# Kernel optimization log

Measured on AMD Instinct MI355X. Metric: run time of the kernel, lower is better.

The kernel has to match this reference:

```python
import jax, jax.numpy as jnp
import numpy as np

NL, D, DI, N, R, K = 32, 256, 512, 16, 16, 4   # layers, d_model, d_inner, d_state, dt_rank, d_conv
V, FF, BATCH, L = 4096, 1024, 32, 256


def _mamba_layer(x, p):
    # x: (B, L, D). One pre-norm Mamba block with residual: x + mamba(LN(x)).
    ln_w, ln_b, in_w, cw, cb, xp_w, dtw, dtb, A_log, Dskip, out_w = p
    mu = x.mean(-1, keepdims=True)
    var = ((x - mu) ** 2).mean(-1, keepdims=True)
    h = (x - mu) / jnp.sqrt(var + 1e-5) * ln_w + ln_b
    xz = jnp.einsum('bld,ed->ble', h, in_w)            # (B, L, 2*DI)
    xm, z = jnp.split(xz, 2, axis=-1)
    seq = xm.shape[1]
    # causal depthwise conv1d, kernel K, then SiLU
    xpad = jnp.pad(xm, ((0, 0), (K - 1, 0), (0, 0)))
    xc = sum(xpad[:, k:k + seq] * cw[:, k] for k in range(K)) + cb
    xc = jax.nn.silu(xc)
    dbc = jnp.einsum('ble,fe->blf', xc, xp_w)          # (B, L, R+2N)
    dt, Bm, Cm = jnp.split(dbc, [R, R + N], axis=-1)
    dt = jax.nn.softplus(jnp.einsum('blr,er->ble', dt, dtw) + dtb)  # (B, L, DI)
    A = -jnp.exp(A_log)                                # (DI, N)

    def step(hs, inp):
        dt_t, B_t, C_t, x_t = inp                      # (B,DI),(B,N),(B,N),(B,DI)
        dA = jnp.exp(dt_t[..., None] * A)              # (B, DI, N)
        hs = hs * dA + (dt_t * x_t)[..., None] * B_t[:, None, :]
        return hs, jnp.einsum('ben,bn->be', hs, C_t)

    h0 = jnp.zeros((xc.shape[0], DI, N), xc.dtype)
    _, ys = jax.lax.scan(step, h0, (dt.swapaxes(0, 1), Bm.swapaxes(0, 1), Cm.swapaxes(0, 1), xc.swapaxes(0, 1)))
    y = ys.swapaxes(0, 1) + xc * Dskip
    y = y * jax.nn.silu(z)
    return x + jnp.einsum('ble,de->bld', y, out_w)


def _stack_forward(x, params):
    return jax.lax.scan(lambda c, p: (jax.checkpoint(_mamba_layer)(c, p), None), x, params)[0]


def setup_inputs() -> dict:
    key = jax.random.key(0)
    ks = jax.random.split(key, 12)
    rn = lambda k, shape, s=0.02: jax.random.normal(k, shape, jnp.float32) * s
    return {
        'token_ids': jax.random.randint(ks[0], (BATCH, L), 0, V),
        'emb': rn(ks[1], (V, D)),
        'ln_w': jnp.ones((NL, D)), 'ln_b': jnp.zeros((NL, D)),
        'in_proj_w': rn(ks[2], (NL, 2 * DI, D)),
        'conv_w': rn(ks[3], (NL, DI, K), 0.1), 'conv_b': jnp.zeros((NL, DI)),
        'x_proj_w': rn(ks[4], (NL, R + 2 * N, DI)),
        'dt_w': rn(ks[5], (NL, DI, R), 0.1),
        'dt_b': jnp.full((NL, DI), float(np.log(np.expm1(0.01))), jnp.float32),
        'A_log': jnp.broadcast_to(jnp.log(jnp.arange(1, N + 1, dtype=jnp.float32)), (NL, DI, N)) + 0.0,
        'Dskip': jnp.ones((NL, DI)),
        'out_proj_w': rn(ks[6], (NL, D, DI)),
        'W1': rn(ks[7], (FF, D)), 'b1': jnp.zeros((FF,)),
        'W2': rn(ks[8], (V, FF)), 'b2': jnp.zeros((V,)),
    }


def reference(token_ids, emb, ln_w, ln_b, in_proj_w, conv_w, conv_b, x_proj_w, dt_w, dt_b, A_log, Dskip, out_proj_w, W1, b1, W2, b2):
    x = emb[token_ids]                                  # (B, L, D)
    params = (ln_w, ln_b, in_proj_w, conv_w, conv_b, x_proj_w, dt_w, dt_b, A_log, Dskip, out_proj_w)
    x = _stack_forward(x, params)                       # 32 stacked Mamba blocks
    h = jax.nn.relu(x @ W1.T + b1)
    return h @ W2.T + b2                                # (B, L, V) logits
```

## Files before the change

kernel.cpp:

```cpp
#include <hip/hip_runtime.h>
#include <hip/hip_bf16.h>
#include <cstdint>
#include <cstddef>


typedef __bf16 v8bf __attribute__((ext_vector_type(8)));
typedef float  v4f  __attribute__((ext_vector_type(4)));

__device__ __forceinline__ void async_copy16(const void* g, void* l) {
  __builtin_amdgcn_global_load_lds((const __attribute__((address_space(1))) void*)g,
                                   (__attribute__((address_space(3))) void*)l, 16, 0, 0);
}

__device__ __forceinline__ float bf(__bf16 v) { return (float)v; }

constexpr size_t OFF_WIN  = 0;
constexpr size_t OFF_WXP  = 16777216;
constexpr size_t OFF_WOUT = 18350080;
constexpr size_t OFF_WW1  = 26738688;
constexpr size_t OFF_WW2  = 27262976;
constexpr size_t OFF_X    = 35651584;
constexpr size_t OFF_H    = 44040192;
constexpr size_t OFF_XZ   = 48234496;
constexpr size_t OFF_XC   = 65011712;
constexpr size_t OFF_DBC  = 73400320;
constexpr size_t OFF_Y    = 74973184;
constexpr size_t OFF_PART = 83361792;
constexpr size_t OFF_PROD = 91750400;

__global__ __launch_bounds__(256)
void f2b_multi(const float* __restrict__ s0, const float* __restrict__ s1,
               const float* __restrict__ s2, const float* __restrict__ s3,
               const float* __restrict__ s4, char* __restrict__ ws) {
  size_t i = (size_t)blockIdx.x * 256 + threadIdx.x;
  if (i < 8388608) { ((__bf16*)(ws + OFF_WIN))[i] = (__bf16)s0[i]; return; }
  i -= 8388608;
  if (i < 786432)  { ((__bf16*)(ws + OFF_WXP))[i] = (__bf16)s1[i]; return; }
  i -= 786432;
  if (i < 4194304) { ((__bf16*)(ws + OFF_WOUT))[i] = (__bf16)s2[i]; return; }
  i -= 4194304;
  if (i < 262144)  { ((__bf16*)(ws + OFF_WW1))[i] = (__bf16)s3[i]; return; }
  i -= 262144;
  ((__bf16*)(ws + OFF_WW2))[i] = (__bf16)s4[i];
}

__global__ __launch_bounds__(256) void f2b_k(const float* __restrict__ X,
                                             __bf16* __restrict__ O) {
  size_t i = (size_t)blockIdx.x * 256 + threadIdx.x;
  O[i] = (__bf16)X[i];
}

__global__ __launch_bounds__(256)
void embed_ln_k(const int* __restrict__ tok, const float* __restrict__ emb,
                const float* __restrict__ w, const float* __restrict__ b,
                float* __restrict__ X, __bf16* __restrict__ H) {
  int row = blockIdx.x;
  int t   = threadIdx.x;
  float v = emb[(size_t)tok[row] * 256 + t];
  X[(size_t)row * 256 + t] = v;
  float s = v, q = v * v;
  #pragma unroll
  for (int o = 32; o > 0; o >>= 1) { s += __shfl_xor(s, o); q += __shfl_xor(q, o); }
  __shared__ float ss[4], qq[4];
  int wv = t >> 6;
  if ((t & 63) == 0) { ss[wv] = s; qq[wv] = q; }
  __syncthreads();
  s = ss[0] + ss[1] + ss[2] + ss[3];
  q = qq[0] + qq[1] + qq[2] + qq[3];
  float mu  = s * (1.f / 256.f);
  float var = q * (1.f / 256.f) - mu * mu;
  float r   = rsqrtf(var + 1e-5f);
  H[(size_t)row * 256 + t] = (__bf16)((v - mu) * r * w[t] + b[t]);
}

template <int EPI>
__global__ __launch_bounds__(256, 2)
void gemm_bt(const __bf16* __restrict__ A, const __bf16* __restrict__ W,
             void* outp, const float* __restrict__ bias, int M, int N, int K) {
  __shared__ __align__(16) __bf16 sA[128 * 32];
  __shared__ __align__(16) __bf16 sB[128 * 32];
  const int tid  = threadIdx.x;
  const int bm0  = blockIdx.y << 7;
  const int bn0  = blockIdx.x << 7;
  const int lane = tid & 63;
  const int wv   = tid >> 6;
  const int wm   = (wv >> 1) << 6;
  const int wn   = (wv & 1) << 6;
  const int lr   = lane & 15;
  const int lk   = lane >> 4;

  v4f acc[4][4] = {};

  const int r0 = tid >> 2;
  const int c0 = (tid & 3) << 3;
  const int wbase = (tid & ~63) << 3;

  const __bf16* gA0 = A + (size_t)(bm0 + r0) * K + c0;
  const __bf16* gA1 = A + (size_t)(bm0 + 64 + r0) * K + c0;
  const __bf16* gB0 = W + (size_t)(bn0 + r0) * K + c0;
  const __bf16* gB1 = W + (size_t)(bn0 + 64 + r0) * K + c0;

  for (int kk = 0; kk < K; kk += 32) {
    async_copy16(gA0 + kk, sA + wbase);
    async_copy16(gA1 + kk, sA + 2048 + wbase);
    async_copy16(gB0 + kk, sB + wbase);
    async_copy16(gB1 + kk, sB + 2048 + wbase);
    __syncthreads();
    v8bf af[4], bfr[4];
    #pragma unroll
    for (int i = 0; i < 4; ++i)
      af[i] = *(const v8bf*)(sA + ((wm + i * 16 + lr) << 5) + (lk << 3));
    #pragma unroll
    for (int j = 0; j < 4; ++j)
      bfr[j] = *(const v8bf*)(sB + ((wn + j * 16 + lr) << 5) + (lk << 3));
    #pragma unroll
    for (int i = 0; i < 4; ++i)
      #pragma unroll
      for (int j = 0; j < 4; ++j)
        acc[i][j] = __builtin_amdgcn_mfma_f32_16x16x32_bf16(af[i], bfr[j], acc[i][j], 0, 0, 0);
    __syncthreads();
  }

  #pragma unroll
  for (int i = 0; i < 4; ++i) {
    #pragma unroll
    for (int j = 0; j < 4; ++j) {
      int gc = bn0 + wn + j * 16 + lr;
      #pragma unroll
      for (int v = 0; v < 4; ++v) {
        int gr = bm0 + wm + i * 16 + (lk << 2) + v;
        float val = acc[i][j][v];
        size_t idx = (size_t)gr * N + gc;
        if (EPI == 0) {
          ((__bf16*)outp)[idx] = (__bf16)val;
        } else if (EPI == 1) {
          val += bias[gc]; val = fmaxf(val, 0.f);
          ((__bf16*)outp)[idx] = (__bf16)val;
        } else {
          ((float*)outp)[idx] = val + bias[gc];
        }
      }
    }
  }
}

__global__ __launch_bounds__(192, 2)
void convxproj_k(const __bf16* __restrict__ XZ, const float* __restrict__ cw,
                 const float* __restrict__ cb, const __bf16* __restrict__ Wxp,
                 __bf16* __restrict__ XC, float* __restrict__ DBC) {
  __shared__ __align__(16) __bf16 sA[32 * 32];
  __shared__ __align__(16) __bf16 sB[48 * 32];
  const int tid  = threadIdx.x;
  const int bl0  = blockIdx.x << 5;
  const int lane = tid & 63, wv = tid >> 6;
  const int lr = lane & 15, lk = lane >> 4;
  v4f acc[2] = {};

  const int ar = tid >> 2;
  const int ac = (tid & 3) << 3;
  const int bl = bl0 + ar;
  const int l  = bl & 255;

  for (int kk = 0; kk < 512; kk += 32) {
    async_copy16(Wxp + (size_t)(tid >> 2) * 512 + ((tid & 3) << 3) + kk,
                 sB + ((tid & ~63) << 3));
    if (tid < 128) {
      const int e = kk + ac;
      float a[8];
      #pragma unroll
      for (int j = 0; j < 8; ++j) a[j] = cb[e + j];
      #pragma unroll
      for (int k = 0; k < 4; ++k) {
        if (l + k >= 3) {
          const v8bf xv = *(const v8bf*)(XZ + (size_t)(bl + k - 3) * 1024 + e);
          #pragma unroll
          for (int j = 0; j < 8; ++j) a[j] += bf(xv[j]) * cw[(e + j) * 4 + k];
        }
      }
      v8bf outv;
      #pragma unroll
      for (int j = 0; j < 8; ++j) {
        float s = a[j] / (1.f + __expf(-a[j]));
        outv[j] = (__bf16)s;
      }
      *(v8bf*)(sA + ar * 32 + ac) = outv;
      *(v8bf*)(XC + (size_t)bl * 512 + e) = outv;
    }
    __syncthreads();
    v8bf af[2], bfr;
    #pragma unroll
    for (int i = 0; i < 2; ++i)
      af[i] = *(const v8bf*)(sA + ((i * 16 + lr) << 5) + (lk << 3));
    bfr = *(const v8bf*)(sB + ((wv * 16 + lr) << 5) + (lk << 3));
    #pragma unroll
    for (int i = 0; i < 2; ++i)
      acc[i] = __builtin_amdgcn_mfma_f32_16x16x32_bf16(af[i], bfr, acc[i], 0, 0, 0);
    __syncthreads();
  }
  const int gc = wv * 16 + lr;
  #pragma unroll
  for (int i = 0; i < 2; ++i)
    #pragma unroll
    for (int v = 0; v < 4; ++v) {
      int gr = bl0 + i * 16 + (lk << 2) + v;
      DBC[(size_t)gr * 48 + gc] = acc[i][v];
    }
}

__global__ __launch_bounds__(256, 2)
void scan_pass1(const float* __restrict__ DBC, const __bf16* __restrict__ XC,
                const float* __restrict__ dtw, const float* __restrict__ dtb,
                const float* __restrict__ Alog,
                float* __restrict__ PART, float* __restrict__ PROD) {
  const int e = blockIdx.x * 256 + threadIdx.x;
  const int b = blockIdx.y;
  const int c = blockIdx.z;
  float Arow[16], Wdt[16];
  #pragma unroll
  for (int n = 0; n < 16; ++n) {
    Arow[n] = -__expf(Alog[e * 16 + n]);
    Wdt[n]  = dtw[e * 16 + n];
  }
  const float bias = dtb[e];
  float part[16], prod[16];
  #pragma unroll
  for (int n = 0; n < 16; ++n) { part[n] = 0.f; prod[n] = 1.f; }
  const int bl0 = b * 256 + c * 32;
  for (int tt = 0; tt < 32; ++tt) {
    const v4f* dp = (const v4f*)(DBC + (size_t)(bl0 + tt) * 48);
    v4f d0 = dp[0], d1 = dp[1], d2 = dp[2], d3 = dp[3];
    v4f bv0 = dp[4], bv1 = dp[5], bv2 = dp[6], bv3 = dp[7];
    float dtv = bias;
    #pragma unroll
    for (int r = 0; r < 4; ++r)
      dtv += d0[r] * Wdt[r] + d1[r] * Wdt[r + 4] + d2[r] * Wdt[r + 8] + d3[r] * Wdt[r + 12];
    dtv = (dtv > 20.f) ? dtv : log1pf(__expf(dtv));
    float x = bf(XC[(size_t)(bl0 + tt) * 512 + e]);
    float dtx = dtv * x;
    float Bv[16];
    #pragma unroll
    for (int r = 0; r < 4; ++r) { Bv[r] = bv0[r]; Bv[r+4] = bv1[r]; Bv[r+8] = bv2[r]; Bv[r+12] = bv3[r]; }
    #pragma unroll
    for (int n = 0; n < 16; ++n) {
      float dA = __expf(dtv * Arow[n]);
      part[n] = part[n] * dA + dtx * Bv[n];
      prod[n] *= dA;
    }
  }
  size_t o = (((size_t)c * 32 + b) * 512 + e) * 16;
  #pragma unroll
  for (int n = 0; n < 16; ++n) { PART[o + n] = part[n]; PROD[o + n] = prod[n]; }
}

__global__ __launch_bounds__(256, 2)
void scan_pass2(const float* __restrict__ DBC, const __bf16* __restrict__ XC,
                const __bf16* __restrict__ XZ,
                const float* __restrict__ dtw, const float* __restrict__ dtb,
                const float* __restrict__ Alog, const float* __restrict__ Dskip,
                const float* __restrict__ PART, const float* __restrict__ PROD,
                __bf16* __restrict__ Y) {
  const int e = blockIdx.x * 256 + threadIdx.x;
  const int b = blockIdx.y;
  const int c = blockIdx.z;
  float Arow[16], Wdt[16];
  #pragma unroll
  for (int n = 0; n < 16; ++n) {
    Arow[n] = -__expf(Alog[e * 16 + n]);
    Wdt[n]  = dtw[e * 16 + n];
  }
  const float bias = dtb[e];
  const float Dsk  = Dskip[e];
  float h[16];
  #pragma unroll
  for (int n = 0; n < 16; ++n) h[n] = 0.f;
  for (int cc = 0; cc < c; ++cc) {
    size_t o = (((size_t)cc * 32 + b) * 512 + e) * 16;
    const v4f* pp = (const v4f*)(PART + o);
    const v4f* qq = (const v4f*)(PROD + o);
    #pragma unroll
    for (int r = 0; r < 4; ++r) {
      v4f p = pp[r], q = qq[r];
      #pragma unroll
      for (int v = 0; v < 4; ++v) h[r * 4 + v] = q[v] * h[r * 4 + v] + p[v];
    }
  }
  const int bl0 = b * 256 + c * 32;
  for (int tt = 0; tt < 32; ++tt) {
    const v4f* dp = (const v4f*)(DBC + (size_t)(bl0 + tt) * 48);
    v4f d0 = dp[0], d1 = dp[1], d2 = dp[2], d3 = dp[3];
    v4f bv0 = dp[4], bv1 = dp[5], bv2 = dp[6], bv3 = dp[7];
    v4f cv0 = dp[8], cv1 = dp[9], cv2 = dp[10], cv3 = dp[11];
    float dtv = bias;
    #pragma unroll
    for (int r = 0; r < 4; ++r)
      dtv += d0[r] * Wdt[r] + d1[r] * Wdt[r + 4] + d2[r] * Wdt[r + 8] + d3[r] * Wdt[r + 12];
    dtv = (dtv > 20.f) ? dtv : log1pf(__expf(dtv));
    float x = bf(XC[(size_t)(bl0 + tt) * 512 + e]);
    float dtx = dtv * x;
    float Bv[16], Cv[16];
    #pragma unroll
    for (int r = 0; r < 4; ++r) {
      Bv[r] = bv0[r]; Bv[r+4] = bv1[r]; Bv[r+8] = bv2[r]; Bv[r+12] = bv3[r];
      Cv[r] = cv0[r]; Cv[r+4] = cv1[r]; Cv[r+8] = cv2[r]; Cv[r+12] = cv3[r];
    }
    float y = 0.f;
    #pragma unroll
    for (int n = 0; n < 16; ++n) {
      float dA = __expf(dtv * Arow[n]);
      h[n] = h[n] * dA + dtx * Bv[n];
      y += h[n] * Cv[n];
    }
    float z  = bf(XZ[(size_t)(bl0 + tt) * 1024 + 512 + e]);
    float sg = z / (1.f + __expf(-z));
    Y[(size_t)(bl0 + tt) * 512 + e] = (__bf16)((y + x * Dsk) * sg);
  }
}

__global__ __launch_bounds__(256, 2)
void gemm_out_ln_k(const __bf16* __restrict__ Yb, const __bf16* __restrict__ Wout,
                   const float* __restrict__ lnw, const float* __restrict__ lnb,
                   float* __restrict__ X, __bf16* __restrict__ H) {
  __shared__ __align__(16) __bf16 sA[32 * 32];
  __shared__ __align__(16) __bf16 sB[256 * 32];
  __shared__ float sSum[4][32], sSq[4][32];
  const int tid  = threadIdx.x;
  const int bm0  = blockIdx.x << 5;
  const int lane = tid & 63, wv = tid >> 6;
  const int lr = lane & 15, lk = lane >> 4;
  v4f acc[2][4] = {};

  const int ar = tid >> 2;
  const int ac = (tid & 3) << 3;

  for (int kk = 0; kk < 512; kk += 32) {
    if (tid < 128)
      async_copy16(Yb + (size_t)(bm0 + ar) * 512 + ac + kk, sA + ((tid & ~63) << 3));
    #pragma unroll
    for (int j = 0; j < 4; ++j) {
      int ch = j * 256 + tid;
      async_copy16(Wout + (size_t)(ch >> 2) * 512 + ((ch & 3) << 3) + kk,
                   sB + ((j * 256 + (tid & ~63)) << 3));
    }
    __syncthreads();
    v8bf af[2], bfr[4];
    #pragma unroll
    for (int i = 0; i < 2; ++i)
      af[i] = *(const v8bf*)(sA + ((i * 16 + lr) << 5) + (lk << 3));
    #pragma unroll
    for (int j = 0; j < 4; ++j)
      bfr[j] = *(const v8bf*)(sB + ((wv * 64 + j * 16 + lr) << 5) + (lk << 3));
    #pragma unroll
    for (int i = 0; i < 2; ++i)
      #pragma unroll
      for (int j = 0; j < 4; ++j)
        acc[i][j] = __builtin_amdgcn_mfma_f32_16x16x32_bf16(af[i], bfr[j], acc[i][j], 0, 0, 0);
    __syncthreads();
  }

  float s2[2][4], q2[2][4];
  #pragma unroll
  for (int i = 0; i < 2; ++i)
    #pragma unroll
    for (int v = 0; v < 4; ++v) {
      int gr = bm0 + i * 16 + (lk << 2) + v;
      float s = 0.f, q = 0.f;
      #pragma unroll
      for (int j = 0; j < 4; ++j) {
        int gc = wv * 64 + j * 16 + lr;
        float val = X[(size_t)gr * 256 + gc] + acc[i][j][v];
        acc[i][j][v] = val;
        s += val; q += val * val;
      }
      #pragma unroll
      for (int o = 8; o > 0; o >>= 1) { s += __shfl_xor(s, o); q += __shfl_xor(q, o); }
      s2[i][v] = s; q2[i][v] = q;
    }
  if (lr == 0) {
    #pragma unroll
    for (int i = 0; i < 2; ++i)
      #pragma unroll
      for (int v = 0; v < 4; ++v) {
        int row = i * 16 + (lk << 2) + v;
        sSum[wv][row] = s2[i][v];
        sSq[wv][row]  = q2[i][v];
      }
  }
  __syncthreads();
  #pragma unroll
  for (int i = 0; i < 2; ++i)
    #pragma unroll
    for (int v = 0; v < 4; ++v) {
      int row = i * 16 + (lk << 2) + v;
      float S = sSum[0][row] + sSum[1][row] + sSum[2][row] + sSum[3][row];
      float Q = sSq[0][row]  + sSq[1][row]  + sSq[2][row]  + sSq[3][row];
      float mu  = S * (1.f / 256.f);
      float var = Q * (1.f / 256.f) - mu * mu;
      float rinv = rsqrtf(var + 1e-5f);
      int gr = bm0 + row;
      #pragma unroll
      for (int j = 0; j < 4; ++j) {
        int gc = wv * 64 + j * 16 + lr;
        float val = acc[i][j][v];
        X[(size_t)gr * 256 + gc] = val;
        H[(size_t)gr * 256 + gc] = (__bf16)((val - mu) * rinv * lnw[gc] + lnb[gc]);
      }
    }
}

extern "C" void kernel_launch(void* const* d_in, const int* in_sizes, int n_in,
                              void* d_out, int out_size, void* d_ws, size_t ws_size,
                              hipStream_t stream) {
  const int*   tok  = (const int*)d_in[0];
  const float* emb  = (const float*)d_in[1];
  const float* lnw  = (const float*)d_in[2];
  const float* lnb  = (const float*)d_in[3];
  const float* inw  = (const float*)d_in[4];
  const float* cw   = (const float*)d_in[5];
  const float* cb   = (const float*)d_in[6];
  const float* xpw  = (const float*)d_in[7];
  const float* dtw  = (const float*)d_in[8];
  const float* dtb  = (const float*)d_in[9];
  const float* alog = (const float*)d_in[10];
  const float* dsk  = (const float*)d_in[11];
  const float* outw = (const float*)d_in[12];
  const float* W1   = (const float*)d_in[13];
  const float* b1   = (const float*)d_in[14];
  const float* W2   = (const float*)d_in[15];
  const float* b2   = (const float*)d_in[16];

  char* ws = (char*)d_ws;
  __bf16* WIN  = (__bf16*)(ws + OFF_WIN);
  __bf16* WXP  = (__bf16*)(ws + OFF_WXP);
  __bf16* WOUT = (__bf16*)(ws + OFF_WOUT);
  __bf16* WW1  = (__bf16*)(ws + OFF_WW1);
  __bf16* WW2  = (__bf16*)(ws + OFF_WW2);
  float*  X    = (float*)(ws + OFF_X);
  __bf16* H    = (__bf16*)(ws + OFF_H);
  __bf16* XZ   = (__bf16*)(ws + OFF_XZ);
  __bf16* XC   = (__bf16*)(ws + OFF_XC);
  float*  DBC  = (float*)(ws + OFF_DBC);
  __bf16* Y    = (__bf16*)(ws + OFF_Y);
  float*  PART = (float*)(ws + OFF_PART);
  float*  PROD = (float*)(ws + OFF_PROD);
  __bf16* XB   = (__bf16*)(ws + OFF_PART);
  __bf16* HH   = (__bf16*)(ws + OFF_PROD);

  f2b_multi<<<69632, 256, 0, stream>>>(inw, xpw, outw, W1, W2, ws);
  embed_ln_k<<<8192, 256, 0, stream>>>(tok, emb, lnw, lnb, X, H);

  for (int l = 0; l < 32; ++l) {
    const __bf16* inw_l  = WIN  + (size_t)l * 1024 * 256;
    const float*  cw_l   = cw   + (size_t)l * 512 * 4;
    const float*  cb_l   = cb   + (size_t)l * 512;
    const __bf16* xpw_l  = WXP  + (size_t)l * 48 * 512;
    const float*  dtw_l  = dtw  + (size_t)l * 512 * 16;
    const float*  dtb_l  = dtb  + (size_t)l * 512;
    const float*  alog_l = alog + (size_t)l * 512 * 16;
    const float*  dsk_l  = dsk  + (size_t)l * 512;
    const __bf16* outw_l = WOUT + (size_t)l * 256 * 512;
    const int lnx = (l + 1 < 32) ? l + 1 : 31;

    gemm_bt<0><<<dim3(8, 64), 256, 0, stream>>>(H, inw_l, XZ, nullptr, 8192, 1024, 256);
    convxproj_k<<<256, 192, 0, stream>>>(XZ, cw_l, cb_l, xpw_l, XC, DBC);
    scan_pass1<<<dim3(2, 32, 7), 256, 0, stream>>>(DBC, XC, dtw_l, dtb_l, alog_l, PART, PROD);
    scan_pass2<<<dim3(2, 32, 8), 256, 0, stream>>>(DBC, XC, XZ, dtw_l, dtb_l, alog_l, dsk_l,
                                                   PART, PROD, Y);
    gemm_out_ln_k<<<256, 256, 0, stream>>>(Y, outw_l, lnw + (size_t)lnx * 256,
                                           lnb + (size_t)lnx * 256, X, H);
  }

  f2b_k<<<8192, 256, 0, stream>>>(X, XB);
  gemm_bt<1><<<dim3(8, 64), 256, 0, stream>>>(XB, WW1, HH, b1, 8192, 1024, 256);
  gemm_bt<2><<<dim3(32, 64), 256, 0, stream>>>(HH, WW2, (float*)d_out, b2, 8192, 4096, 1024);
}
```

Baseline: 4.926 ms.

## Fuse conv+xproj+scan pass1 and scan pass2+out-proj+LN into two kernels

Result: faster. 4.236 ms (-14.0%).

```diff
diff --git a/kernel.cpp b/kernel.cpp
--- a/kernel.cpp
+++ b/kernel.cpp
@@ -22,9 +22,7 @@
 constexpr size_t OFF_X    = 35651584;
 constexpr size_t OFF_H    = 44040192;
 constexpr size_t OFF_XZ   = 48234496;
-constexpr size_t OFF_XC   = 65011712;
 constexpr size_t OFF_DBC  = 73400320;
-constexpr size_t OFF_Y    = 74973184;
 constexpr size_t OFF_PART = 83361792;
 constexpr size_t OFF_PROD = 91750400;
 
@@ -144,149 +142,182 @@
   }
 }
 
-__global__ __launch_bounds__(192, 2)
-void convxproj_k(const __bf16* __restrict__ XZ, const float* __restrict__ cw,
-                 const float* __restrict__ cb, const __bf16* __restrict__ Wxp,
-                 __bf16* __restrict__ XC, float* __restrict__ DBC) {
-  __shared__ __align__(16) __bf16 sA[32 * 32];
-  __shared__ __align__(16) __bf16 sB[48 * 32];
-  const int tid  = threadIdx.x;
-  const int bl0  = blockIdx.x << 5;
-  const int lane = tid & 63, wv = tid >> 6;
-  const int lr = lane & 15, lk = lane >> 4;
-  v4f acc[2] = {};
-
-  const int ar = tid >> 2;
-  const int ac = (tid & 3) << 3;
-  const int bl = bl0 + ar;
-  const int l  = bl & 255;
-
-  for (int kk = 0; kk < 512; kk += 32) {
-    async_copy16(Wxp + (size_t)(tid >> 2) * 512 + ((tid & 3) << 3) + kk,
-                 sB + ((tid & ~63) << 3));
-    if (tid < 128) {
-      const int e = kk + ac;
+__global__ __launch_bounds__(512, 2)
+void convscan1_k(const __bf16* __restrict__ XZ,
+                 const float* __restrict__ cw, const float* __restrict__ cb,
+                 const __bf16* __restrict__ Wxp,
+                 const float* __restrict__ dtw, const float* __restrict__ dtb,
+                 const float* __restrict__ Alog,
+                 float* __restrict__ DBC,
+                 float* __restrict__ PART, float* __restrict__ PROD) {
+  __shared__ __align__(16) __bf16 sXC[32 * 512];
+  __shared__ __align__(16) float  sDBC[32 * 48];
+  const int tid = threadIdx.x;
+  const int c   = blockIdx.x >> 5;
+  const int b   = blockIdx.x & 31;
+  const int bl0 = b * 256 + c * 32;
+
+  {
+    const int r  = tid >> 4;
+    const int ec = tid & 15;
+    #pragma unroll
+    for (int j = 0; j < 4; ++j) {
+      const int e = (ec << 3) + (j << 7);
+      v4f cw4[8];
+      #pragma unroll
+      for (int jj = 0; jj < 8; ++jj) cw4[jj] = *(const v4f*)(cw + (size_t)(e + jj) * 4);
       float a[8];
       #pragma unroll
-      for (int j = 0; j < 8; ++j) a[j] = cb[e + j];
+      for (int jj = 0; jj < 8; ++jj) a[jj] = cb[e + jj];
       #pragma unroll
       for (int k = 0; k < 4; ++k) {
-        if (l + k >= 3) {
-          const v8bf xv = *(const v8bf*)(XZ + (size_t)(bl + k - 3) * 1024 + e);
+        if (c > 0 || r + k >= 3) {
+          const v8bf xv = *(const v8bf*)(XZ + (size_t)(bl0 + r + k - 3) * 1024 + e);
           #pragma unroll
-          for (int j = 0; j < 8; ++j) a[j] += bf(xv[j]) * cw[(e + j) * 4 + k];
+          for (int jj = 0; jj < 8; ++jj) a[jj] += bf(xv[jj]) * cw4[jj][k];
         }
       }
       v8bf outv;
       #pragma unroll
-      for (int j = 0; j < 8; ++j) {
-        float s = a[j] / (1.f + __expf(-a[j]));
-        outv[j] = (__bf16)s;
+      for (int jj = 0; jj < 8; ++jj) {
+        float s = a[jj] / (1.f + __expf(-a[jj]));
+        outv[jj] = (__bf16)s;
       }
-      *(v8bf*)(sA + ar * 32 + ac) = outv;
-      *(v8bf*)(XC + (size_t)bl * 512 + e) = outv;
-    }
-    __syncthreads();
-    v8bf af[2], bfr;
+      const int cbk = (e >> 3) ^ (r & 7);
+      *(v8bf*)(sXC + r * 512 + (cbk << 3)) = outv;
+    }
+  }
+  __syncthreads();
+
+  if (tid < 192) {
+    const int w = tid >> 6, lane = tid & 63, lr = lane & 15, lk = lane >> 4;
+    v4f acc[2] = {};
+    for (int kk = 0; kk < 512; kk += 32) {
+      const v8bf bfr = *(const v8bf*)(Wxp + (size_t)(w * 16 + lr) * 512 + kk + (lk << 3));
+      #pragma unroll
+      for (int i = 0; i < 2; ++i) {
+        const int row = i * 16 + lr;
+        const int cbk = (((kk >> 3) + lk) ^ (row & 7));
+        const v8bf af = *(const v8bf*)(sXC + row * 512 + (cbk << 3));
+        acc[i] = __builtin_amdgcn_mfma_f32_16x16x32_bf16(af, bfr, acc[i], 0, 0, 0);
+      }
+    }
+    const int gc = w * 16 + lr;
     #pragma unroll
     for (int i = 0; i < 2; ++i)
-      af[i] = *(const v8bf*)(sA + ((i * 16 + lr) << 5) + (lk << 3));
-    bfr = *(const v8bf*)(sB + ((wv * 16 + lr) << 5) + (lk << 3));
-    #pragma unroll
-    for (int i = 0; i < 2; ++i)
-      acc[i] = __builtin_amdgcn_mfma_f32_16x16x32_bf16(af[i], bfr, acc[i], 0, 0, 0);
-    __syncthreads();
-  }
-  const int gc = wv * 16 + lr;
-  #pragma unroll
-  for (int i = 0; i < 2; ++i)
-    #pragma unroll
-    for (int v = 0; v < 4; ++v) {
-      int gr = bl0 + i * 16 + (lk << 2) + v;
-      DBC[(size_t)gr * 48 + gc] = acc[i][v];
-    }
-}
-
-__global__ __launch_bounds__(256, 2)
-void scan_pass1(const float* __restrict__ DBC, const __bf16* __restrict__ XC,
-                const float* __restrict__ dtw, const float* __restrict__ dtb,
-                const float* __restrict__ Alog,
-                float* __restrict__ PART, float* __restrict__ PROD) {
-  const int e = blockIdx.x * 256 + threadIdx.x;
-  const int b = blockIdx.y;
-  const int c = blockIdx.z;
-  float Arow[16], Wdt[16];
-  #pragma unroll
-  for (int n = 0; n < 16; ++n) {
-    Arow[n] = -__expf(Alog[e * 16 + n]);
-    Wdt[n]  = dtw[e * 16 + n];
-  }
-  const float bias = dtb[e];
-  float part[16], prod[16];
-  #pragma unroll
-  for (int n = 0; n < 16; ++n) { part[n] = 0.f; prod[n] = 1.f; }
-  const int bl0 = b * 256 + c * 32;
-  for (int tt = 0; tt < 32; ++tt) {
-    const v4f* dp = (const v4f*)(DBC + (size_t)(bl0 + tt) * 48);
-    v4f d0 = dp[0], d1 = dp[1], d2 = dp[2], d3 = dp[3];
-    v4f bv0 = dp[4], bv1 = dp[5], bv2 = dp[6], bv3 = dp[7];
-    float dtv = bias;
-    #pragma unroll
-    for (int r = 0; r < 4; ++r)
-      dtv += d0[r] * Wdt[r] + d1[r] * Wdt[r + 4] + d2[r] * Wdt[r + 8] + d3[r] * Wdt[r + 12];
-    dtv = (dtv > 20.f) ? dtv : log1pf(__expf(dtv));
-    float x = bf(XC[(size_t)(bl0 + tt) * 512 + e]);
-    float dtx = dtv * x;
-    float Bv[16];
-    #pragma unroll
-    for (int r = 0; r < 4; ++r) { Bv[r] = bv0[r]; Bv[r+4] = bv1[r]; Bv[r+8] = bv2[r]; Bv[r+12] = bv3[r]; }
+      #pragma unroll
+      for (int v = 0; v < 4; ++v)
+        sDBC[(i * 16 + (lk << 2) + v) * 48 + gc] = acc[i][v];
+  }
+  __syncthreads();
+
+  if (tid < 384)
+    *(v4f*)(DBC + (size_t)bl0 * 48 + tid * 4) = *(const v4f*)(sDBC + tid * 4);
+
+  if (c < 7) {
+    const int e = tid;
+    float Arow2[16], Wdt[16];
     #pragma unroll
     for (int n = 0; n < 16; ++n) {
-      float dA = __expf(dtv * Arow[n]);
-      part[n] = part[n] * dA + dtx * Bv[n];
-      prod[n] *= dA;
-    }
-  }
-  size_t o = (((size_t)c * 32 + b) * 512 + e) * 16;
-  #pragma unroll
-  for (int n = 0; n < 16; ++n) { PART[o + n] = part[n]; PROD[o + n] = prod[n]; }
-}
-
-__global__ __launch_bounds__(256, 2)
-void scan_pass2(const float* __restrict__ DBC, const __bf16* __restrict__ XC,
-                const __bf16* __restrict__ XZ,
+      Arow2[n] = -1.4426950408889634f * __expf(Alog[(size_t)e * 16 + n]);
+      Wdt[n]   = dtw[(size_t)e * 16 + n];
+    }
+    const float bias = dtb[e];
+    float part[16], prod[16];
+    #pragma unroll
+    for (int n = 0; n < 16; ++n) { part[n] = 0.f; prod[n] = 1.f; }
+    for (int tt = 0; tt < 32; ++tt) {
+      const v4f* dp = (const v4f*)(sDBC + tt * 48);
+      v4f d0 = dp[0], d1 = dp[1], d2 = dp[2], d3 = dp[3];
+      v4f bv0 = dp[4], bv1 = dp[5], bv2 = dp[6], bv3 = dp[7];
+      float dtv = bias;
+      #pragma unroll
+      for (int r = 0; r < 4; ++r)
+        dtv += d0[r] * Wdt[r] + d1[r] * Wdt[r + 4] + d2[r] * Wdt[r + 8] + d3[r] * Wdt[r + 12];
+      dtv = (dtv > 20.f) ? dtv : log1pf(__expf(dtv));
+      const float x = bf(sXC[tt * 512 + (((e >> 3) ^ (tt & 7)) << 3) + (e & 7)]);
+      const float dtx = dtv * x;
+      float Bv[16];
+      #pragma unroll
+      for (int r = 0; r < 4; ++r) { Bv[r] = bv0[r]; Bv[r+4] = bv1[r]; Bv[r+8] = bv2[r]; Bv[r+12] = bv3[r]; }
+      #pragma unroll
+      for (int n = 0; n < 16; ++n) {
+        const float dA = exp2f(dtv * Arow2[n]);
+        part[n] = part[n] * dA + dtx * Bv[n];
+        prod[n] *= dA;
+      }
+    }
+    const size_t o = (((size_t)c * 32 + b) * 512 + e) * 16;
+    #pragma unroll
+    for (int rq = 0; rq < 4; ++rq) {
+      v4f p, q;
+      #pragma unroll
+      for (int v = 0; v < 4; ++v) { p[v] = part[rq * 4 + v]; q[v] = prod[rq * 4 + v]; }
+      *(v4f*)(PART + o + rq * 4) = p;
+      *(v4f*)(PROD + o + rq * 4) = q;
+    }
+  }
+}
+
+__global__ __launch_bounds__(512, 2)
+void scan2out_k(const __bf16* __restrict__ XZ,
+                const float* __restrict__ cw, const float* __restrict__ cb,
+                const float* __restrict__ DBC,
                 const float* __restrict__ dtw, const float* __restrict__ dtb,
                 const float* __restrict__ Alog, const float* __restrict__ Dskip,
                 const float* __restrict__ PART, const float* __restrict__ PROD,
-                __bf16* __restrict__ Y) {
-  const int e = blockIdx.x * 256 + threadIdx.x;
-  const int b = blockIdx.y;
-  const int c = blockIdx.z;
-  float Arow[16], Wdt[16];
+                const __bf16* __restrict__ Wout,
+                const float* __restrict__ lnw, const float* __restrict__ lnb,
+                float* __restrict__ X, __bf16* __restrict__ H) {
+  __shared__ __align__(16) __bf16 sY[32 * 520];
+  __shared__ __align__(16) __bf16 sB[256 * 32];
+  __shared__ float sSum[4][32], sSq[4][32];
+  const int tid = threadIdx.x;
+  const int c   = blockIdx.x >> 5;
+  const int b   = blockIdx.x & 31;
+  const int bl0 = b * 256 + c * 32;
+  const int e   = tid;
+
+  float Arow2[16], Wdt[16];
   #pragma unroll
   for (int n = 0; n < 16; ++n) {
-    Arow[n] = -__expf(Alog[e * 16 + n]);
-    Wdt[n]  = dtw[e * 16 + n];
+    Arow2[n] = -1.4426950408889634f * __expf(Alog[(size_t)e * 16 + n]);
+    Wdt[n]   = dtw[(size_t)e * 16 + n];
   }
   const float bias = dtb[e];
   const float Dsk  = Dskip[e];
+  const v4f   cwv  = *(const v4f*)(cw + (size_t)e * 4);
+  const float cbe  = cb[e];
+
   float h[16];
   #pragma unroll
   for (int n = 0; n < 16; ++n) h[n] = 0.f;
   for (int cc = 0; cc < c; ++cc) {
-    size_t o = (((size_t)cc * 32 + b) * 512 + e) * 16;
-    const v4f* pp = (const v4f*)(PART + o);
-    const v4f* qq = (const v4f*)(PROD + o);
-    #pragma unroll
-    for (int r = 0; r < 4; ++r) {
-      v4f p = pp[r], q = qq[r];
-      #pragma unroll
-      for (int v = 0; v < 4; ++v) h[r * 4 + v] = q[v] * h[r * 4 + v] + p[v];
-    }
-  }
-  const int bl0 = b * 256 + c * 32;
+    const size_t o = (((size_t)cc * 32 + b) * 512 + e) * 16;
+    #pragma unroll
+    for (int rq = 0; rq < 4; ++rq) {
+      const v4f p = *(const v4f*)(PART + o + rq * 4);
+      const v4f q = *(const v4f*)(PROD + o + rq * 4);
+      #pragma unroll
+      for (int v = 0; v < 4; ++v) h[rq * 4 + v] = q[v] * h[rq * 4 + v] + p[v];
+    }
+  }
+
+  float w0 = 0.f, w1 = 0.f, w2 = 0.f;
+  if (c > 0) {
+    w0 = bf(XZ[(size_t)(bl0 - 3) * 1024 + e]);
+    w1 = bf(XZ[(size_t)(bl0 - 2) * 1024 + e]);
+    w2 = bf(XZ[(size_t)(bl0 - 1) * 1024 + e]);
+  }
+
+  #pragma unroll 2
   for (int tt = 0; tt < 32; ++tt) {
-    const v4f* dp = (const v4f*)(DBC + (size_t)(bl0 + tt) * 48);
+    const float xt = bf(XZ[(size_t)(bl0 + tt) * 1024 + e]);
+    float a = cbe + w0 * cwv[0] + w1 * cwv[1] + w2 * cwv[2] + xt * cwv[3];
+    const float x = a / (1.f + __expf(-a));
+    w0 = w1; w1 = w2; w2 = xt;
+    const float* dpf = DBC + (size_t)(bl0 + tt) * 48;
+    const v4f* dp = (const v4f*)dpf;
     v4f d0 = dp[0], d1 = dp[1], d2 = dp[2], d3 = dp[3];
     v4f bv0 = dp[4], bv1 = dp[5], bv2 = dp[6], bv3 = dp[7];
     v4f cv0 = dp[8], cv1 = dp[9], cv2 = dp[10], cv3 = dp[11];
@@ -295,8 +326,7 @@
     for (int r = 0; r < 4; ++r)
       dtv += d0[r] * Wdt[r] + d1[r] * Wdt[r + 4] + d2[r] * Wdt[r + 8] + d3[r] * Wdt[r + 12];
     dtv = (dtv > 20.f) ? dtv : log1pf(__expf(dtv));
-    float x = bf(XC[(size_t)(bl0 + tt) * 512 + e]);
-    float dtx = dtv * x;
+    const float dtx = dtv * x;
     float Bv[16], Cv[16];
     #pragma unroll
     for (int r = 0; r < 4; ++r) {
@@ -306,105 +336,77 @@
     float y = 0.f;
     #pragma unroll
     for (int n = 0; n < 16; ++n) {
-      float dA = __expf(dtv * Arow[n]);
+      const float dA = exp2f(dtv * Arow2[n]);
       h[n] = h[n] * dA + dtx * Bv[n];
       y += h[n] * Cv[n];
     }
-    float z  = bf(XZ[(size_t)(bl0 + tt) * 1024 + 512 + e]);
-    float sg = z / (1.f + __expf(-z));
-    Y[(size_t)(bl0 + tt) * 512 + e] = (__bf16)((y + x * Dsk) * sg);
-  }
-}
-
-__global__ __launch_bounds__(256, 2)
-void gemm_out_ln_k(const __bf16* __restrict__ Yb, const __bf16* __restrict__ Wout,
-                   const float* __restrict__ lnw, const float* __restrict__ lnb,
-                   float* __restrict__ X, __bf16* __restrict__ H) {
-  __shared__ __align__(16) __bf16 sA[32 * 32];
-  __shared__ __align__(16) __bf16 sB[256 * 32];
-  __shared__ float sSum[4][32], sSq[4][32];
-  const int tid  = threadIdx.x;
-  const int bm0  = blockIdx.x << 5;
-  const int lane = tid & 63, wv = tid >> 6;
-  const int lr = lane & 15, lk = lane >> 4;
-  v4f acc[2][4] = {};
-
-  const int ar = tid >> 2;
-  const int ac = (tid & 3) << 3;
-
+    const float z  = bf(XZ[(size_t)(bl0 + tt) * 1024 + 512 + e]);
+    const float sg = z / (1.f + __expf(-z));
+    sY[tt * 520 + e] = (__bf16)((y + x * Dsk) * sg);
+  }
+  __syncthreads();
+
+  const int w = tid >> 6, lane = tid & 63, lr = lane & 15, lk = lane >> 4;
+  const int wm = (w & 1) << 4;
+  const int wn = (w >> 1) << 6;
+  v4f acc[4] = {};
   for (int kk = 0; kk < 512; kk += 32) {
-    if (tid < 128)
-      async_copy16(Yb + (size_t)(bm0 + ar) * 512 + ac + kk, sA + ((tid & ~63) << 3));
+    async_copy16(Wout + (size_t)(tid >> 2) * 512 + ((tid & 3) << 3) + kk,
+                 sB + ((tid & ~63) << 3));
+    async_copy16(Wout + (size_t)(128 + (tid >> 2)) * 512 + ((tid & 3) << 3) + kk,
+                 sB + 4096 + ((tid & ~63) << 3));
+    __syncthreads();
+    const v8bf af = *(const v8bf*)(sY + (wm + lr) * 520 + kk + (lk << 3));
     #pragma unroll
     for (int j = 0; j < 4; ++j) {
-      int ch = j * 256 + tid;
-      async_copy16(Wout + (size_t)(ch >> 2) * 512 + ((ch & 3) << 3) + kk,
-                   sB + ((j * 256 + (tid & ~63)) << 3));
+      const v8bf bfr = *(const v8bf*)(sB + ((wn + j * 16 + lr) << 5) + (lk << 3));
+      acc[j] = __builtin_amdgcn_mfma_f32_16x16x32_bf16(af, bfr, acc[j], 0, 0, 0);
     }
     __syncthreads();
-    v8bf af[2], bfr[4];
-    #pragma unroll
-    for (int i = 0; i < 2; ++i)
-      af[i] = *(const v8bf*)(sA + ((i * 16 + lr) << 5) + (lk << 3));
-    #pragma unroll
-    for (int j = 0; j < 4; ++j)
-      bfr[j] = *(const v8bf*)(sB + ((wv * 64 + j * 16 + lr) << 5) + (lk << 3));
-    #pragma unroll
-    for (int i = 0; i < 2; ++i)
-      #pragma unroll
-      for (int j = 0; j < 4; ++j)
-        acc[i][j] = __builtin_amdgcn_mfma_f32_16x16x32_bf16(af[i], bfr[j], acc[i][j], 0, 0, 0);
-    __syncthreads();
-  }
-
-  float s2[2][4], q2[2][4];
-  #pragma unroll
-  for (int i = 0; i < 2; ++i)
+  }
+
+  float s2[4], q2[4];
+  #pragma unroll
+  for (int v = 0; v < 4; ++v) {
+    const int gr = bl0 + wm + (lk << 2) + v;
+    float s = 0.f, q = 0.f;
+    #pragma unroll
+    for (int j = 0; j < 4; ++j) {
+      const int gc = wn + j * 16 + lr;
+      float val = X[(size_t)gr * 256 + gc] + acc[j][v];
+      acc[j][v] = val;
+      s += val; q += val * val;
+    }
+    #pragma unroll
+    for (int o = 8; o > 0; o >>= 1) { s += __shfl_xor(s, o); q += __shfl_xor(q, o); }
+    s2[v] = s; q2[v] = q;
+  }
+  if (lr == 0) {
     #pragma unroll
     for (int v = 0; v < 4; ++v) {
-      int gr = bm0 + i * 16 + (lk << 2) + v;
-      float s = 0.f, q = 0.f;
-      #pragma unroll
-      for (int j = 0; j < 4; ++j) {
-        int gc = wv * 64 + j * 16 + lr;
-        float val = X[(size_t)gr * 256 + gc] + acc[i][j][v];
-        acc[i][j][v] = val;
-        s += val; q += val * val;
-      }
-      #pragma unroll
-      for (int o = 8; o > 0; o >>= 1) { s += __shfl_xor(s, o); q += __shfl_xor(q, o); }
-      s2[i][v] = s; q2[i][v] = q;
-    }
-  if (lr == 0) {
-    #pragma unroll
-    for (int i = 0; i < 2; ++i)
-      #pragma unroll
-      for (int v = 0; v < 4; ++v) {
-        int row = i * 16 + (lk << 2) + v;
-        sSum[wv][row] = s2[i][v];
-        sSq[wv][row]  = q2[i][v];
-      }
+      const int row = wm + (lk << 2) + v;
+      sSum[w >> 1][row] = s2[v];
+      sSq[w >> 1][row]  = q2[v];
+    }
   }
   __syncthreads();
   #pragma unroll
-  for (int i = 0; i < 2; ++i)
-    #pragma unroll
-    for (int v = 0; v < 4; ++v) {
-      int row = i * 16 + (lk << 2) + v;
-      float S = sSum[0][row] + sSum[1][row] + sSum[2][row] + sSum[3][row];
-      float Q = sSq[0][row]  + sSq[1][row]  + sSq[2][row]  + sSq[3][row];
-      float mu  = S * (1.f / 256.f);
-      float var = Q * (1.f / 256.f) - mu * mu;
-      float rinv = rsqrtf(var + 1e-5f);
-      int gr = bm0 + row;
-      #pragma unroll
-      for (int j = 0; j < 4; ++j) {
-        int gc = wv * 64 + j * 16 + lr;
-        float val = acc[i][j][v];
-        X[(size_t)gr * 256 + gc] = val;
-        H[(size_t)gr * 256 + gc] = (__bf16)((val - mu) * rinv * lnw[gc] + lnb[gc]);
-      }
-    }
+  for (int v = 0; v < 4; ++v) {
+    const int row = wm + (lk << 2) + v;
+    const float S = sSum[0][row] + sSum[1][row] + sSum[2][row] + sSum[3][row];
+    const float Q = sSq[0][row]  + sSq[1][row]  + sSq[2][row]  + sSq[3][row];
+    const float mu  = S * (1.f / 256.f);
+    const float var = Q * (1.f / 256.f) - mu * mu;
+    const float rinv = rsqrtf(var + 1e-5f);
+    const int gr = bl0 + row;
+    #pragma unroll
+    for (int j = 0; j < 4; ++j) {
+      const int gc = wn + j * 16 + lr;
+      const float val = acc[j][v];
+      X[(size_t)gr * 256 + gc] = val;
+      H[(size_t)gr * 256 + gc] = (__bf16)((val - mu) * rinv * lnw[gc] + lnb[gc]);
+    }
+  }
 }
 
 extern "C" void kernel_launch(void* const* d_in, const int* in_sizes, int n_in,
@@ -429,21 +431,19 @@
   const float* b2   = (const float*)d_in[16];
 
   char* ws = (char*)d_ws;
-  __bf16* WIN  = (__bf16*)(ws + OFF_WIN);
-  __bf16* WXP  = (__bf16*)(ws + OFF_WXP);
-  __bf16* WOUT = (__bf16*)(ws + OFF_WOUT);
-  __bf16* WW1  = (__bf16*)(ws + OFF_WW1);
-  __bf16* WW2  = (__bf16*)(ws + OFF_WW2);
-  float*  X    = (float*)(ws + OFF_X);
-  __bf16* H    = (__bf16*)(ws + OFF_H);
-  __bf16* XZ   = (__bf16*)(ws + OFF_XZ);
-  __bf16* XC   = (__bf16*)(ws + OFF_XC);
-  float*  DBC  = (float*)(ws + OFF_DBC);
-  __bf16* Y    = (__bf16*)(ws + OFF_Y);
-  float*  PART = (float*)(ws + OFF_PART);
-  float*  PROD = (float*)(ws + OFF_PROD);
-  __bf16* XB   = (__bf16*)(ws + OFF_PART);
-  __bf16* HH   = (__bf16*)(ws + OFF_PROD);
+  __bf16* WIN   = (__bf16*)(ws + OFF_WIN);
+  __bf16* WXP   = (__bf16*)(ws + OFF_WXP);
+  __bf16* WOUT  = (__bf16*)(ws + OFF_WOUT);
+  __bf16* WW1   = (__bf16*)(ws + OFF_WW1);
+  __bf16* WW2   = (__bf16*)(ws + OFF_WW2);
+  float*  X     = (float*)(ws + OFF_X);
+  __bf16* H     = (__bf16*)(ws + OFF_H);
+  __bf16* XZ    = (__bf16*)(ws + OFF_XZ);
+  float*  DBC   = (float*)(ws + OFF_DBC);
+  float*  PART  = (float*)(ws + OFF_PART);
+  float*  PROD  = (float*)(ws + OFF_PROD);
+  __bf16* XB    = (__bf16*)(ws + OFF_PART);
+  __bf16* HH    = (__bf16*)(ws + OFF_PROD);
 
   f2b_multi<<<69632, 256, 0, stream>>>(inw, xpw, outw, W1, W2, ws);
   embed_ln_k<<<8192, 256, 0, stream>>>(tok, emb, lnw, lnb, X, H);
@@ -461,12 +461,12 @@
     const int lnx = (l + 1 < 32) ? l + 1 : 31;
 
     gemm_bt<0><<<dim3(8, 64), 256, 0, stream>>>(H, inw_l, XZ, nullptr, 8192, 1024, 256);
-    convxproj_k<<<256, 192, 0, stream>>>(XZ, cw_l, cb_l, xpw_l, XC, DBC);
-    scan_pass1<<<dim3(2, 32, 7), 256, 0, stream>>>(DBC, XC, dtw_l, dtb_l, alog_l, PART, PROD);
-    scan_pass2<<<dim3(2, 32, 8), 256, 0, stream>>>(DBC, XC, XZ, dtw_l, dtb_l, alog_l, dsk_l,
-                                                   PART, PROD, Y);
-    gemm_out_ln_k<<<256, 256, 0, stream>>>(Y, outw_l, lnw + (size_t)lnx * 256,
-                                           lnb + (size_t)lnx * 256, X, H);
+    convscan1_k<<<256, 512, 0, stream>>>(XZ, cw_l, cb_l, xpw_l, dtw_l, dtb_l,
+                                         alog_l, DBC, PART, PROD);
+    scan2out_k<<<256, 512, 0, stream>>>(XZ, cw_l, cb_l, DBC, dtw_l, dtb_l,
+                                        alog_l, dsk_l, PART, PROD, outw_l,
+                                        lnw + (size_t)lnx * 256,
+                                        lnb + (size_t)lnx * 256, X, H);
   }
 
   f2b_k<<<8192, 256, 0, stream>>>(X, XB);
```
